# Optimization experiments

Hardware: AMD Instinct MI355X
Metric: run time of the kernel (lower is better)

Reference implementation:

```python
import jax, jax.numpy as jnp
import numpy as np

TOP_K = 2  # standard top-2 MoE gating


def setup_inputs() -> dict:
    key = jax.random.key(0)
    k1, k2, k3, k4 = jax.random.split(key, 4)
    T, D, E = 8192, 1024, 8
    x = jax.random.normal(k1, (T, D), dtype=jnp.float32)
    Wg = jax.random.normal(k2, (D, E), dtype=jnp.float32) * (1.0 / np.sqrt(D))
    We = jax.random.normal(k3, (E, D, D), dtype=jnp.float32) * (1.0 / np.sqrt(D))
    be = jax.random.normal(k4, (E, D), dtype=jnp.float32) * 0.02
    return {"x": x, "Wg": Wg, "We": We, "be": be}


def reference(x, Wg, We, be):
    # x: [T, D]; Wg: [D, E]; We: [E, D, D]; be: [E, D]
    T = x.shape[0]
    logits = x @ Wg                          # [T, E]
    probs = jax.nn.softmax(logits, axis=-1)  # [T, E]
    top_v, top_i = jax.lax.top_k(probs, TOP_K)           # [T, K]
    top_v = top_v / jnp.sum(top_v, axis=-1, keepdims=True)
    # dense combine weights [T, E] (zero for non-selected experts)
    cw = jnp.zeros_like(probs).at[jnp.arange(T)[:, None], top_i].add(top_v)
    # per-expert GEMM over all tokens (E is small), then masked combine
    h = jnp.einsum('td,edf->etf', x, We) + be[:, None, :]  # [E, T, D]
    h = jax.nn.relu(h)
    y = jnp.einsum('te,etf->tf', cw, h)                    # [T, D]
    return y
```

## Files before the change

### kernel.cpp

```cpp
#include <hip/hip_runtime.h>

#define T_TOKENS 8192
#define DMODEL   1024
#define NEXP     8

#define BM 128
#define BN 128
#define BK 64
#define NSTEP (DMODEL / BK)

typedef float f32x4  __attribute__((ext_vector_type(4)));
typedef short short8 __attribute__((ext_vector_type(8)));

__device__ __forceinline__ unsigned short f32_to_bf16(float f) {
    unsigned int u = __builtin_bit_cast(unsigned int, f);
    unsigned int r = 0x7FFFu + ((u >> 16) & 1u);
    return (unsigned short)((u + r) >> 16);
}

__global__ __launch_bounds__(256)
void prep(const float* __restrict__ x, const float* __restrict__ Wg,
          const float* __restrict__ We,
          unsigned short* __restrict__ xb, unsigned short* __restrict__ wt,
          int* __restrict__ top_e, float* __restrict__ top_w) {
    __shared__ unsigned short tile[64][72];
    const int bid = blockIdx.x;

    if (bid < 2048) {
        const int wave = threadIdx.x >> 6;
        const int lane = threadIdx.x & 63;
        const int t = bid * 4 + wave;

        float lg[8];
        #pragma unroll
        for (int e = 0; e < 8; ++e) lg[e] = 0.0f;

        const float* xr = x + (size_t)t * DMODEL;
        unsigned short* xo = xb + (size_t)t * DMODEL;

        #pragma unroll
        for (int j = 0; j < 4; ++j) {
            const int d = j * 256 + lane * 4;
            float4 xv = *reinterpret_cast<const float4*>(xr + d);
            ushort4 o;
            o.x = f32_to_bf16(xv.x);
            o.y = f32_to_bf16(xv.y);
            o.z = f32_to_bf16(xv.z);
            o.w = f32_to_bf16(xv.w);
            *reinterpret_cast<ushort4*>(xo + d) = o;
            const float xs[4] = {xv.x, xv.y, xv.z, xv.w};
            #pragma unroll
            for (int c = 0; c < 4; ++c) {
                const float4 wlo = *reinterpret_cast<const float4*>(Wg + (size_t)(d + c) * 8);
                const float4 whi = *reinterpret_cast<const float4*>(Wg + (size_t)(d + c) * 8 + 4);
                lg[0] += xs[c] * wlo.x;  lg[1] += xs[c] * wlo.y;
                lg[2] += xs[c] * wlo.z;  lg[3] += xs[c] * wlo.w;
                lg[4] += xs[c] * whi.x;  lg[5] += xs[c] * whi.y;
                lg[6] += xs[c] * whi.z;  lg[7] += xs[c] * whi.w;
            }
        }
        #pragma unroll
        for (int off = 1; off < 64; off <<= 1) {
            #pragma unroll
            for (int e = 0; e < 8; ++e) lg[e] += __shfl_xor(lg[e], off);
        }

        if (lane == 0) {
            int i1 = 0; float v1 = lg[0];
            #pragma unroll
            for (int e = 1; e < 8; ++e) if (lg[e] > v1) { v1 = lg[e]; i1 = e; }
            int i2 = -1; float v2 = -1e30f;
            #pragma unroll
            for (int e = 0; e < 8; ++e) if (e != i1 && lg[e] > v2) { v2 = lg[e]; i2 = e; }
            const float w1 = 1.0f / (1.0f + __expf(v2 - v1));
            top_e[t] = i1 | (i2 << 4);
            top_w[t] = w1;
        }
    } else {
        const int idx = bid - 2048;
        const int e   = idx >> 8;
        const int rem = idx & 255;
        const int d0  = (rem >> 4) * 64;
        const int f0  = (rem & 15) * 64;
        const float* src = We + ((size_t)e * DMODEL + d0) * DMODEL + f0;
        #pragma unroll
        for (int j = 0; j < 4; ++j) {
            const int ix = j * 256 + threadIdx.x;
            const int dl = ix >> 4;
            const int fq = ix & 15;
            float4 v = *reinterpret_cast<const float4*>(src + (size_t)dl * DMODEL + fq * 4);
            tile[fq * 4 + 0][dl] = f32_to_bf16(v.x);
            tile[fq * 4 + 1][dl] = f32_to_bf16(v.y);
            tile[fq * 4 + 2][dl] = f32_to_bf16(v.z);
            tile[fq * 4 + 3][dl] = f32_to_bf16(v.w);
        }
        __syncthreads();
        unsigned short* dst = wt + ((size_t)e * DMODEL + f0) * DMODEL + d0;
        #pragma unroll
        for (int j = 0; j < 4; ++j) {
            const int ix = j * 256 + threadIdx.x;
            const int fl = ix >> 4;
            const int dq = ix & 15;
            ushort4 v = *reinterpret_cast<const ushort4*>(&tile[fl][dq * 4]);
            *reinterpret_cast<ushort4*>(dst + (size_t)fl * DMODEL + dq * 4) = v;
        }
    }
}

__global__ __launch_bounds__(256)
void compact(const int* __restrict__ top_e, const float* __restrict__ top_w,
             int* __restrict__ counts, int* __restrict__ toks,
             float* __restrict__ wgts, int* __restrict__ rows) {
    const int e    = blockIdx.x;
    const int c    = blockIdx.y;
    const int tid  = threadIdx.x;
    const int wave = tid >> 6;
    const int lane = tid & 63;

    __shared__ int sm[256];
    __shared__ int red[4];
    __shared__ int ws[4];

    int mc = 0;
    const int4* tp = reinterpret_cast<const int4*>(top_e) + tid * 8;
    #pragma unroll
    for (int i = 0; i < 8; ++i) {
        int4 v = tp[i];
        mc += (((v.x & 15) == e) || (((v.x >> 4) & 15) == e)) ? 1 : 0;
        mc += (((v.y & 15) == e) || (((v.y >> 4) & 15) == e)) ? 1 : 0;
        mc += (((v.z & 15) == e) || (((v.z >> 4) & 15) == e)) ? 1 : 0;
        mc += (((v.w & 15) == e) || (((v.w >> 4) & 15) == e)) ? 1 : 0;
    }
    sm[tid] = mc;
    __syncthreads();

    int v = (tid < c * 8) ? sm[tid] : 0;
    #pragma unroll
    for (int off = 1; off < 64; off <<= 1) v += __shfl_xor(v, off);
    if (lane == 0) red[wave] = v;
    __syncthreads();
    const int base = red[0] + red[1] + red[2] + red[3];

    const int t  = c * 256 + tid;
    const int te = top_e[t];
    const int e1 = te & 15;
    const int e2 = (te >> 4) & 15;
    const bool m = (e1 == e) || (e2 == e);
    const unsigned long long b = __ballot(m);
    const int pos_in_wave = __popcll(b & ((1ull << lane) - 1ull));
    if (lane == 0) ws[wave] = __popcll(b);
    __syncthreads();

    int woff = base;
    #pragma unroll
    for (int i = 0; i < 4; ++i) if (i < wave) woff += ws[i];

    if (m) {
        const int pos = woff + pos_in_wave;
        const float w1 = top_w[t];
        toks[e * T_TOKENS + pos] = t;
        wgts[e * T_TOKENS + pos] = (e1 == e) ? w1 : 1.0f - w1;
        rows[t * 2 + ((e1 == e) ? 0 : 1)] = e * T_TOKENS + pos;
    }
    if (c == 31 && tid == 0)
        counts[e] = base + ws[0] + ws[1] + ws[2] + ws[3];
}

__global__ __launch_bounds__(256)
void expert_gemm(const unsigned short* __restrict__ xb,
                 const unsigned short* __restrict__ wt,
                 const float* __restrict__ be,
                 const int* __restrict__ counts,
                 const int* __restrict__ toks,
                 const float* __restrict__ wgts,
                 unsigned short* __restrict__ hpart) {
    const int flat = blockIdx.x + 64 * (blockIdx.y + 8 * blockIdx.z);
    const int e    = flat & 7;
    const int rest = flat >> 3;
    const int fy   = rest & 7;
    const int tx   = rest >> 3;

    const int cnt = counts[e];
    const int p0  = tx * BM;
    if (p0 >= cnt) return;
    const int f0  = fy * BN;

    __shared__ unsigned short lds_w[BN * BK];
    __shared__ unsigned short lds_x[BM * BK];
    __shared__ int   tok_s[BM];
    __shared__ float wgt_s[BM];

    const int tid  = threadIdx.x;
    const int wave = tid >> 6;
    const int lane = tid & 63;

    if (tid < BM) {
        int p = p0 + tid;
        if (p < cnt) {
            tok_s[tid] = toks[e * T_TOKENS + p];
            wgt_s[tid] = wgts[e * T_TOKENS + p];
        } else {
            tok_s[tid] = 0;
            wgt_s[tid] = 0.0f;
        }
    }
    __syncthreads();

    const char* wsrc[4];
    const char* xsrc[4];
    #pragma unroll
    for (int s = 0; s < 4; ++s) {
        const int q    = wave * 4 + s;
        const int row  = q * 8 + (lane >> 3);
        const int scol = ((lane & 7) << 4) ^ ((row & 7) << 4);
        wsrc[s] = (const char*)wt + ((size_t)(e * DMODEL + f0 + row) * DMODEL) * 2 + scol;
        xsrc[s] = (const char*)xb + ((size_t)tok_s[row] * DMODEL) * 2 + scol;
    }

    f32x4 acc[4][4] = {};

    const int wf = (wave & 1) * 64;
    const int wp = (wave >> 1) * 64;

    #pragma unroll 1
    for (int t = 0; t < NSTEP; ++t) {
        const size_t ko = (size_t)t * BK * 2;
        #pragma unroll
        for (int s = 0; s < 4; ++s) {
            __builtin_amdgcn_global_load_lds(
                (const __attribute__((address_space(1))) void*)(wsrc[s] + ko),
                (__attribute__((address_space(3))) void*)((char*)lds_w + (wave * 4 + s) * 1024),
                16, 0, 0);
            __builtin_amdgcn_global_load_lds(
                (const __attribute__((address_space(1))) void*)(xsrc[s] + ko),
                (__attribute__((address_space(3))) void*)((char*)lds_x + (wave * 4 + s) * 1024),
                16, 0, 0);
        }
        __syncthreads();

        #pragma unroll
        for (int kk = 0; kk < 2; ++kk) {
            short8 afr[4], bfr[4];
            #pragma unroll
            for (int mi = 0; mi < 4; ++mi) {
                const int row = wf + mi * 16 + (lane & 15);
                const int kb  = (kk * 64 + ((lane >> 4) << 4)) ^ ((row & 7) << 4);
                afr[mi] = *(const short8*)((const char*)lds_w + row * 128 + kb);
            }
            #pragma unroll
            for (int ni = 0; ni < 4; ++ni) {
                const int row = wp + ni * 16 + (lane & 15);
                const int kb  = (kk * 64 + ((lane >> 4) << 4)) ^ ((row & 7) << 4);
                bfr[ni] = *(const short8*)((const char*)lds_x + row * 128 + kb);
            }
            #pragma unroll
            for (int mi = 0; mi < 4; ++mi)
                #pragma unroll
                for (int ni = 0; ni < 4; ++ni)
                    asm("v_mfma_f32_16x16x32_bf16 %0, %1, %2, %0"
                        : "+a"(acc[mi][ni])
                        : "v"(afr[mi]), "v"(bfr[ni]));
        }
        __syncthreads();
    }

    #pragma unroll
    for (int ni = 0; ni < 4; ++ni) {
        const int pl = wp + ni * 16 + (lane & 15);
        const int p  = p0 + pl;
        if (p >= cnt) continue;
        const float w = wgt_s[pl];
        unsigned short* hr = hpart + (size_t)(e * T_TOKENS + p) * DMODEL + f0 + wf;
        #pragma unroll
        for (int mi = 0; mi < 4; ++mi) {
            const int fb = mi * 16 + ((lane >> 4) << 2);
            const float* ber = be + (size_t)e * DMODEL + f0 + wf + fb;
            ushort4 o;
            float v0 = acc[mi][ni][0] + ber[0]; v0 = v0 > 0.f ? v0 : 0.f;
            float v1 = acc[mi][ni][1] + ber[1]; v1 = v1 > 0.f ? v1 : 0.f;
            float v2 = acc[mi][ni][2] + ber[2]; v2 = v2 > 0.f ? v2 : 0.f;
            float v3 = acc[mi][ni][3] + ber[3]; v3 = v3 > 0.f ? v3 : 0.f;
            o.x = f32_to_bf16(v0 * w);
            o.y = f32_to_bf16(v1 * w);
            o.z = f32_to_bf16(v2 * w);
            o.w = f32_to_bf16(v3 * w);
            *reinterpret_cast<ushort4*>(hr + fb) = o;
        }
    }
}

__global__ __launch_bounds__(256)
void combine(const unsigned short* __restrict__ hpart,
             const int* __restrict__ rows,
             float* __restrict__ y) {
    const int t = blockIdx.x;
    const int r0 = rows[t * 2 + 0];
    const int r1 = rows[t * 2 + 1];
    const int f = threadIdx.x * 4;
    ushort4 a = *reinterpret_cast<const ushort4*>(hpart + (size_t)r0 * DMODEL + f);
    ushort4 b = *reinterpret_cast<const ushort4*>(hpart + (size_t)r1 * DMODEL + f);
    float4 o;
    o.x = __builtin_bit_cast(float, (unsigned)a.x << 16) + __builtin_bit_cast(float, (unsigned)b.x << 16);
    o.y = __builtin_bit_cast(float, (unsigned)a.y << 16) + __builtin_bit_cast(float, (unsigned)b.y << 16);
    o.z = __builtin_bit_cast(float, (unsigned)a.z << 16) + __builtin_bit_cast(float, (unsigned)b.z << 16);
    o.w = __builtin_bit_cast(float, (unsigned)a.w << 16) + __builtin_bit_cast(float, (unsigned)b.w << 16);
    *reinterpret_cast<float4*>(y + (size_t)t * DMODEL + f) = o;
}

extern "C" void kernel_launch(void* const* d_in, const int* in_sizes, int n_in,
                              void* d_out, int out_size, void* d_ws, size_t ws_size,
                              hipStream_t stream) {
    (void)in_sizes; (void)n_in; (void)out_size; (void)ws_size;
    const float* x  = (const float*)d_in[0];
    const float* Wg = (const float*)d_in[1];
    const float* We = (const float*)d_in[2];
    const float* be = (const float*)d_in[3];
    float* y = (float*)d_out;

    char* ws = (char*)d_ws;
    unsigned short* xb     = (unsigned short*)(ws);
    unsigned short* wt     = (unsigned short*)(ws + (16u << 20));
    size_t off = (32u << 20);
    int*   counts = (int*)(ws + off);    off += 1024;
    int*   toks   = (int*)(ws + off);    off += (size_t)NEXP * T_TOKENS * 4;
    float* wgts   = (float*)(ws + off);  off += (size_t)NEXP * T_TOKENS * 4;
    int*   rows   = (int*)(ws + off);    off += (size_t)T_TOKENS * 2 * 4;
    int*   top_e  = (int*)(ws + off);    off += (size_t)T_TOKENS * 4;
    float* top_w  = (float*)(ws + off);
    unsigned short* hpart = (unsigned short*)(ws + (34u << 20));

    prep<<<dim3(4096), 256, 0, stream>>>(x, Wg, We, xb, wt, top_e, top_w);
    compact<<<dim3(NEXP, 32), 256, 0, stream>>>(top_e, top_w, counts, toks, wgts, rows);
    expert_gemm<<<dim3(T_TOKENS / BM, DMODEL / BN, NEXP), 256, 0, stream>>>(
        xb, wt, be, counts, toks, wgts, hpart);
    combine<<<dim3(T_TOKENS), 256, 0, stream>>>(hpart, rows, y);
}
```

Measured before the change: 106.2 us.

## Use MFMA builtin and widen combine kernel loads to 16 bytes

```diff
diff --git a/kernel.cpp b/kernel.cpp
--- a/kernel.cpp
+++ b/kernel.cpp
@@ -257,9 +257,8 @@
             for (int mi = 0; mi < 4; ++mi)
                 #pragma unroll
                 for (int ni = 0; ni < 4; ++ni)
-                    asm("v_mfma_f32_16x16x32_bf16 %0, %1, %2, %0"
-                        : "+a"(acc[mi][ni])
-                        : "v"(afr[mi]), "v"(bfr[ni]));
+                    acc[mi][ni] = __builtin_amdgcn_mfma_f32_16x16x32_bf16(
+                        afr[mi], bfr[ni], acc[mi][ni], 0, 0, 0);
         }
         __syncthreads();
     }
@@ -293,18 +292,25 @@
 void combine(const unsigned short* __restrict__ hpart,
              const int* __restrict__ rows,
              float* __restrict__ y) {
-    const int t = blockIdx.x;
+    const int t = blockIdx.x * 2 + (threadIdx.x >> 7);
+    const int lane128 = threadIdx.x & 127;
     const int r0 = rows[t * 2 + 0];
     const int r1 = rows[t * 2 + 1];
-    const int f = threadIdx.x * 4;
-    ushort4 a = *reinterpret_cast<const ushort4*>(hpart + (size_t)r0 * DMODEL + f);
-    ushort4 b = *reinterpret_cast<const ushort4*>(hpart + (size_t)r1 * DMODEL + f);
-    float4 o;
-    o.x = __builtin_bit_cast(float, (unsigned)a.x << 16) + __builtin_bit_cast(float, (unsigned)b.x << 16);
-    o.y = __builtin_bit_cast(float, (unsigned)a.y << 16) + __builtin_bit_cast(float, (unsigned)b.y << 16);
-    o.z = __builtin_bit_cast(float, (unsigned)a.z << 16) + __builtin_bit_cast(float, (unsigned)b.z << 16);
-    o.w = __builtin_bit_cast(float, (unsigned)a.w << 16) + __builtin_bit_cast(float, (unsigned)b.w << 16);
-    *reinterpret_cast<float4*>(y + (size_t)t * DMODEL + f) = o;
+    const int f = lane128 * 8;
+    uint4 a = *reinterpret_cast<const uint4*>(hpart + (size_t)r0 * DMODEL + f);
+    uint4 b = *reinterpret_cast<const uint4*>(hpart + (size_t)r1 * DMODEL + f);
+    float4 o0, o1;
+    o0.x = __builtin_bit_cast(float, (a.x & 0xFFFFu) << 16) + __builtin_bit_cast(float, (b.x & 0xFFFFu) << 16);
+    o0.y = __builtin_bit_cast(float, (a.x & 0xFFFF0000u))   + __builtin_bit_cast(float, (b.x & 0xFFFF0000u));
+    o0.z = __builtin_bit_cast(float, (a.y & 0xFFFFu) << 16) + __builtin_bit_cast(float, (b.y & 0xFFFFu) << 16);
+    o0.w = __builtin_bit_cast(float, (a.y & 0xFFFF0000u))   + __builtin_bit_cast(float, (b.y & 0xFFFF0000u));
+    o1.x = __builtin_bit_cast(float, (a.z & 0xFFFFu) << 16) + __builtin_bit_cast(float, (b.z & 0xFFFFu) << 16);
+    o1.y = __builtin_bit_cast(float, (a.z & 0xFFFF0000u))   + __builtin_bit_cast(float, (b.z & 0xFFFF0000u));
+    o1.z = __builtin_bit_cast(float, (a.w & 0xFFFFu) << 16) + __builtin_bit_cast(float, (b.w & 0xFFFFu) << 16);
+    o1.w = __builtin_bit_cast(float, (a.w & 0xFFFF0000u))   + __builtin_bit_cast(float, (b.w & 0xFFFF0000u));
+    float* yr = y + (size_t)t * DMODEL + f;
+    *reinterpret_cast<float4*>(yr)     = o0;
+    *reinterpret_cast<float4*>(yr + 4) = o1;
 }
 
 extern "C" void kernel_launch(void* const* d_in, const int* in_sizes, int n_in,
@@ -333,5 +339,5 @@
     compact<<<dim3(NEXP, 32), 256, 0, stream>>>(top_e, top_w, counts, toks, wgts, rows);
     expert_gemm<<<dim3(T_TOKENS / BM, DMODEL / BN, NEXP), 256, 0, stream>>>(
         xb, wt, be, counts, toks, wgts, hpart);
-    combine<<<dim3(T_TOKENS), 256, 0, stream>>>(hpart, rows, y);
-}
+    combine<<<dim3(T_TOKENS / 2), 256, 0, stream>>>(hpart, rows, y);
+}
```

New measurement: 125.7 us. +18.4%, slower.
